# Kernel tuning notes

Hardware: AMD Instinct MI355X
Metric: run time of the kernel (lower is better)

The kernel has to match this reference:

```python
import jax, jax.numpy as jnp
import numpy as np

NUM_GRAPHS = 512
NODES_PER_GRAPH = 152  # hard-coded by reshape(-1, 152*C) in the original forward
DEG = 8
N = NUM_GRAPHS * NODES_PER_GRAPH          # 77824
E = NUM_GRAPHS * NODES_PER_GRAPH * DEG    # 622592
F_IN = 128
HID = 32
HEADS = 6
C = HID * HEADS                           # 192
EPS = 1e-5
NEG_SLOPE = 0.2


def setup_inputs() -> dict:
    key = jax.random.key(0)
    ks = jax.random.split(key, 20)
    x = jax.random.normal(ks[0], (N, F_IN), dtype=jnp.float32)
    # edges are intra-graph: local indices in [0,152) + per-graph offset
    src_l = jax.random.randint(ks[1], (E,), 0, NODES_PER_GRAPH)
    dst_l = jax.random.randint(ks[2], (E,), 0, NODES_PER_GRAPH)
    offs = (jnp.arange(E) // (NODES_PER_GRAPH * DEG)) * NODES_PER_GRAPH
    edge_index = jnp.stack([src_l + offs, dst_l + offs]).astype(jnp.int32)
    batch = (jnp.arange(N) // NODES_PER_GRAPH).astype(jnp.int32)

    def g(k, shape, s=0.05):
        return jax.random.normal(k, shape, dtype=jnp.float32) * s

    return {
        "x": x, "edge_index": edge_index, "batch": batch,
        # GATConv 1: in=128 -> heads=6, d_head=32, concat -> 192
        "W1": g(ks[3], (F_IN, C)), "a_src1": g(ks[4], (HEADS, HID)),
        "a_dst1": g(ks[5], (HEADS, HID)), "b1": jnp.zeros((C,), jnp.float32),
        # GATConv 2: in=192 -> 192
        "W2": g(ks[6], (C, C)), "a_src2": g(ks[7], (HEADS, HID)),
        "a_dst2": g(ks[8], (HEADS, HID)), "b2": jnp.zeros((C,), jnp.float32),
        # GraphNorm 1 / 2: weight, bias, mean_scale (all init like PyG: 1,0,1)
        "gw1": jnp.ones((C,), jnp.float32), "gb1": jnp.zeros((C,), jnp.float32),
        "gms1": jnp.ones((C,), jnp.float32),
        "gw2": jnp.ones((C,), jnp.float32), "gb2": jnp.zeros((C,), jnp.float32),
        "gms2": jnp.ones((C,), jnp.float32),
    }


def _gat_conv(x, W, a_src, a_dst, bias, src, dst):
    # PyG GATConv (concat=True, negative_slope=0.2, add_self_loops already in src/dst)
    h = (x @ W).reshape(N, HEADS, HID)                      # [N,H,D]
    al_s = jnp.einsum('nhd,hd->nh', h, a_src)               # [N,H]
    al_d = jnp.einsum('nhd,hd->nh', h, a_dst)
    e = jax.nn.leaky_relu(al_s[src] + al_d[dst], NEG_SLOPE)  # [E',H]
    # segment softmax over incoming edges of each dst node
    m = jax.ops.segment_max(e, dst, num_segments=N)
    ex = jnp.exp(e - m[dst])
    denom = jax.ops.segment_sum(ex, dst, num_segments=N)
    alpha = ex / denom[dst]                                  # [E',H]
    out = jax.ops.segment_sum(alpha[:, :, None] * h[src], dst, num_segments=N)
    return out.reshape(N, C) + bias


def _graph_norm(x, batch, w, b, ms):
    # PyG GraphNorm: x - mean_scale*mean, normalized by per-graph std
    cnt = jax.ops.segment_sum(jnp.ones((N, 1), x.dtype), batch, num_segments=NUM_GRAPHS)
    mean = jax.ops.segment_sum(x, batch, num_segments=NUM_GRAPHS) / cnt
    out = x - mean[batch] * ms
    var = jax.ops.segment_sum(out * out, batch, num_segments=NUM_GRAPHS) / cnt
    return out / jnp.sqrt(var[batch] + EPS) * w + b


def reference(x, edge_index, batch, W1, a_src1, a_dst1, b1, W2, a_src2, a_dst2, b2,
              gw1, gb1, gms1, gw2, gb2, gms2):
    # add self loops (PyG GATConv default)
    loops = jnp.arange(N, dtype=edge_index.dtype)
    src = jnp.concatenate([edge_index[0], loops])
    dst = jnp.concatenate([edge_index[1], loops])

    h = _gat_conv(x, W1, a_src1, a_dst1, b1, src, dst)
    h = jax.nn.elu(h)
    h = _graph_norm(h, batch, gw1, gb1, gms1)
    # dropout p=0.5 is identity in eval mode
    h = _gat_conv(h, W2, a_src2, a_dst2, b2, src, dst)
    h = jax.nn.elu(h)
    h = _graph_norm(h, batch, gw2, gb2, gms2)
    out = h.reshape(-1, NODES_PER_GRAPH * C)  # [512, 152*192]
    return out  # original returns (x, embedding) where embedding is x itself
```

## Files before the change

kernel.cpp:

```cpp
#include <hip/hip_runtime.h>
#include <stdint.h>

#define NGRAPH 512
#define NPG    152
#define NNODES (NGRAPH*NPG)
#define DEG    8
#define EPG    (NPG*DEG)
#define NEDGE  (NNODES*DEG)
#define CCH    192
#define HEADS  6
#define HID    32
#define NSEG   (NPG+EPG)
#define HSTR   36
#define CNTP   160

typedef __attribute__((ext_vector_type(8))) short short8v;
typedef __attribute__((ext_vector_type(4))) float f32x4;
typedef __attribute__((ext_vector_type(4))) unsigned short ushort4v;

__device__ __forceinline__ unsigned short f2bf(float f){
  union { float f; uint32_t u; } x; x.f = f;
  uint32_t u = x.u;
  return (unsigned short)((u + 0x7fffu + ((u >> 16) & 1u)) >> 16);
}
__device__ __forceinline__ float bitsf(uint32_t b){
  union { uint32_t u; float f; } x; x.u = b; return x.f;
}
__device__ __forceinline__ void gload_lds16(const void* g, void* l){
  __builtin_amdgcn_global_load_lds((const __attribute__((address_space(1))) void*)g,
                                   (__attribute__((address_space(3))) void*)l, 16, 0, 0);
}

__global__ void wprep_all(const float* __restrict__ W1, const float* __restrict__ W2,
                          unsigned short* __restrict__ Wt1, unsigned short* __restrict__ Wt2){
  int idx = blockIdx.x*256 + threadIdx.x;
  if (idx < CCH*128){
    int c = idx >> 7, k = idx & 127;
    Wt1[idx] = f2bf(W1[k*CCH + c]);
  } else if (idx < CCH*(128+192)){
    int j = idx - CCH*128;
    int c = j/192, k = j - c*192;
    Wt2[j] = f2bf(W2[k*CCH + c]);
  }
}

__global__ __launch_bounds__(256) void csr_build(const int* __restrict__ esrc,
    const int* __restrict__ edst, unsigned short* __restrict__ gsrc,
    int* __restrict__ gcnt){
  __shared__ int cnt[256];
  __shared__ int woff[NPG];
  __shared__ __align__(16) unsigned short slots[NSEG];
  const int t = threadIdx.x, g = blockIdx.x, base = g*NPG;

  cnt[t] = (t < NPG) ? 1 : 0;
  __syncthreads();

  int es[5], ed[5];
  #pragma unroll
  for (int u=0;u<5;u++){
    int i = t + u*256;
    if (i < EPG){
      es[u] = esrc[g*EPG + i] - base;
      ed[u] = edst[g*EPG + i] - base;
      atomicAdd(&cnt[ed[u]], 1);
    }
  }
  __syncthreads();
  for (int off=1; off<256; off<<=1){
    int a = cnt[t];
    int b = (t>=off) ? cnt[t-off] : 0;
    __syncthreads();
    cnt[t] = a + b;
    __syncthreads();
  }
  if (t < NPG){
    int st = (t==0) ? 0 : cnt[t-1];
    woff[t] = st;
    gcnt[g*CNTP + t] = st;
  } else if (t < CNTP){
    gcnt[g*CNTP + t] = NSEG;
  }
  __syncthreads();
  #pragma unroll
  for (int u=0;u<5;u++){
    int i = t + u*256;
    if (i < EPG){
      int pos = atomicAdd(&woff[ed[u]], 1);
      slots[pos] = (unsigned short)es[u];
    }
  }
  if (t < NPG){
    int pos = atomicAdd(&woff[t], 1);
    slots[pos] = (unsigned short)t;
  }
  __syncthreads();
  for (int i=t; i<NSEG/8; i+=256)
    *(int4*)(gsrc + (size_t)g*NSEG + i*8) = *(const int4*)&slots[i*8];
}

template<int K, bool A_BF16>
__global__ __launch_bounds__(256) void gemm_mfma(const void* __restrict__ Ap,
    const unsigned short* __restrict__ Bt, unsigned short* __restrict__ H){
  __shared__ unsigned short lA[64*K];
  __shared__ unsigned short lB[96*K];
  const int t  = threadIdx.x;
  const int m0 = blockIdx.x*64, c0 = blockIdx.y*96;

  if (A_BF16){
    const unsigned short* A = (const unsigned short*)Ap + (size_t)m0*K;
    const int CH = 64*K/8;
    for (int i=t; i<CH; i+=256){
      int o   = i*16;
      int row = o / (2*K);
      int db  = o - row*(2*K);
      int sc  = (db>>4) ^ (row&7);
      gload_lds16(A + (size_t)row*K + sc*8, lA + (size_t)(i-(t&63))*8);
    }
  } else {
    const float* A = (const float*)Ap;
    const int KC = K/8;
    for (int i=t; i<64*KC; i+=256){
      int row = i/KC, c8 = i - row*KC;
      const float* p = A + (size_t)(m0+row)*K + c8*8;
      float4 v0 = *(const float4*)p;
      float4 v1 = *(const float4*)(p+4);
      short8v pk;
      pk[0]=(short)f2bf(v0.x); pk[1]=(short)f2bf(v0.y); pk[2]=(short)f2bf(v0.z); pk[3]=(short)f2bf(v0.w);
      pk[4]=(short)f2bf(v1.x); pk[5]=(short)f2bf(v1.y); pk[6]=(short)f2bf(v1.z); pk[7]=(short)f2bf(v1.w);
      *(short8v*)((char*)lA + row*(2*K) + ((c8*16) ^ ((row&7)<<4))) = pk;
    }
  }
  {
    const unsigned short* Bg = Bt + (size_t)c0*K;
    const int CH = 96*K/8;
    for (int i=t; i<CH; i+=256){
      int o   = i*16;
      int row = o / (2*K);
      int db  = o - row*(2*K);
      int sc  = (db>>4) ^ (row&7);
      gload_lds16(Bg + (size_t)row*K + sc*8, lB + (size_t)(i-(t&63))*8);
    }
  }
  __syncthreads();

  const int wid = t>>6, l = t&63;
  const int wr = wid>>1, wc = wid&1;
  const int r16 = l&15, kq = l>>4;
  f32x4 acc[2][3] = {};
  #pragma unroll
  for (int kk=0; kk<K/32; kk++){
    const int chunk = kk*4 + kq;
    short8v af[2], bf[3];
    #pragma unroll
    for (int m=0;m<2;m++){
      int row = wr*32 + m*16 + r16;
      af[m] = *(const short8v*)((const char*)lA + row*(2*K) + ((chunk*16) ^ ((row&7)<<4)));
    }
    #pragma unroll
    for (int n=0;n<3;n++){
      int col = wc*48 + n*16 + r16;
      bf[n] = *(const short8v*)((const char*)lB + col*(2*K) + ((chunk*16) ^ ((col&7)<<4)));
    }
    #pragma unroll
    for (int m=0;m<2;m++)
      #pragma unroll
      for (int n=0;n<3;n++)
        acc[m][n] = __builtin_amdgcn_mfma_f32_16x16x32_bf16(af[m], bf[n], acc[m][n], 0,0,0);
  }
  const int crow = (l>>4)*4;
  #pragma unroll
  for (int m=0;m<2;m++){
    #pragma unroll
    for (int n=0;n<3;n++){
      int colg = c0 + wc*48 + n*16 + r16;
      #pragma unroll
      for (int r=0;r<4;r++){
        int rowg = m0 + wr*32 + m*16 + crow + r;
        H[(size_t)rowg*CCH + colg] = f2bf(acc[m][n][r]);
      }
    }
  }
}

template<bool OUT_BF16>
__global__ __launch_bounds__(256) void gat_edge(
    const unsigned short* __restrict__ H,
    const unsigned short* __restrict__ gsrc, const int* __restrict__ gcnt,
    const float* __restrict__ a_src, const float* __restrict__ a_dst,
    const float* __restrict__ bias, const float* __restrict__ gw,
    const float* __restrict__ gb, const float* __restrict__ gms,
    void* __restrict__ OUTp)
{
  __shared__ float hN[NPG*HSTR];
  __shared__ float als[NPG], ald[NPG];
  __shared__ __align__(16) unsigned short lsrc[NSEG];
  __shared__ __align__(16) int lcnt[CNTP];
  __shared__ float4 ps[8][8];
  __shared__ float4 mred4[8], vred4[8];

  const int t    = threadIdx.x;
  const int g    = blockIdx.x & 511;
  const int hd   = blockIdx.x >> 9;
  const int base = g*NPG;
  const int lane32 = t & 31, grp = t >> 5;

  {
    const unsigned short* gs = gsrc + (size_t)g*NSEG;
    for (int i=t; i<NSEG/8; i+=256)
      gload_lds16(gs + i*8, lsrc + (size_t)(i-(t&63))*8);
    const int* gc = gcnt + (size_t)g*CNTP;
    if (t < CNTP/4)
      gload_lds16(gc + t*4, lcnt + (size_t)(t-(t&63))*4);
  }

  const int c8c = t&3, nb = t>>2;
  const int ab = hd*HID + c8c*8;
  const float4 avs0 = *(const float4*)&a_src[ab];
  const float4 avs1 = *(const float4*)&a_src[ab+4];
  const float4 avd0 = *(const float4*)&a_dst[ab];
  const float4 avd1 = *(const float4*)&a_dst[ab+4];
  #pragma unroll
  for (int it=0; it<3; it++){
    int n = nb + it*64;
    if (n < NPG){
      int4 v = *(const int4*)(H + (size_t)(base+n)*CCH + hd*HID + c8c*8);
      uint32_t w0=(uint32_t)v.x, w1=(uint32_t)v.y, w2=(uint32_t)v.z, w3=(uint32_t)v.w;
      float4 lo = { bitsf(w0<<16), bitsf(w0&0xffff0000u), bitsf(w1<<16), bitsf(w1&0xffff0000u) };
      float4 hi = { bitsf(w2<<16), bitsf(w2&0xffff0000u), bitsf(w3<<16), bitsf(w3&0xffff0000u) };
      float* dst = &hN[n*HSTR + c8c*8];
      *(float4*)dst = lo;
      *(float4*)(dst+4) = hi;
      float s1 = lo.x*avs0.x + lo.y*avs0.y + lo.z*avs0.z + lo.w*avs0.w
               + hi.x*avs1.x + hi.y*avs1.y + hi.z*avs1.z + hi.w*avs1.w;
      float s2 = lo.x*avd0.x + lo.y*avd0.y + lo.z*avd0.z + lo.w*avd0.w
               + hi.x*avd1.x + hi.y*avd1.y + hi.z*avd1.z + hi.w*avd1.w;
      s1 += __shfl_xor(s1, 1); s1 += __shfl_xor(s1, 2);
      s2 += __shfl_xor(s2, 1); s2 += __shfl_xor(s2, 2);
      if (c8c == 0){ als[n] = s1; ald[n] = s2; }
    }
  }
  __syncthreads();

  const int sub = (lane32>>3)&3;
  const int c8  = lane32&7;
  const int o   = grp*4 + sub;
  float4 acc[5]; float den[5]; int stq[5], lnq[5]; float aldn[5];
  #pragma unroll
  for (int q=0;q<5;q++){
    int n = o + q*32;
    int st=0, en=0; float ad=0.f;
    if (n < NPG){ st = lcnt[n]; en = lcnt[n+1]; ad = ald[n]; }
    stq[q]=st; lnq[q]=en-st; aldn[q]=ad;
    acc[q] = float4{0.f,0.f,0.f,0.f}; den[q]=0.f;
  }
  #pragma unroll
  for (int q=0;q<5;q++){
    int st=stq[q], len=lnq[q];
    float ad = aldn[q];
    int rounds = (len+3)>>2;
    for (int r=0;r<rounds;++r){
      #pragma unroll
      for (int u=0;u<4;u++){
        int j = r*4+u;
        int idx = st + ((j<len)? j : 0);
        int s = (int)lsrc[idx];
        float e = als[s] + ad;
        e = (e>0.f) ? e : 0.2f*e;
        float ex = __expf(e);
        if (j>=len) ex = 0.f;
        const float4 hv = *(const float4*)&hN[s*HSTR + c8*4];
        den[q] += ex;
        acc[q].x = fmaf(ex, hv.x, acc[q].x);
        acc[q].y = fmaf(ex, hv.y, acc[q].y);
        acc[q].z = fmaf(ex, hv.z, acc[q].z);
        acc[q].w = fmaf(ex, hv.w, acc[q].w);
      }
    }
  }

  const int cb = hd*HID + c8*4;
  const float4 bs4 = *(const float4*)&bias[cb];
  const float4 gw4 = *(const float4*)&gw[cb];
  const float4 gb4 = *(const float4*)&gb[cb];
  const float4 ms4 = *(const float4*)&gms[cb];

  float4 outv[5];
  float4 psum = {0.f,0.f,0.f,0.f};
  #pragma unroll
  for (int q=0;q<5;q++){
    int n = o + q*32;
    float4 x = {0.f,0.f,0.f,0.f};
    if (n < NPG){
      float inv = 1.f/den[q];
      x.x = acc[q].x*inv + bs4.x;  x.y = acc[q].y*inv + bs4.y;
      x.z = acc[q].z*inv + bs4.z;  x.w = acc[q].w*inv + bs4.w;
      x.x = (x.x>0.f)?x.x:(__expf(x.x)-1.f);
      x.y = (x.y>0.f)?x.y:(__expf(x.y)-1.f);
      x.z = (x.z>0.f)?x.z:(__expf(x.z)-1.f);
      x.w = (x.w>0.f)?x.w:(__expf(x.w)-1.f);
      psum.x+=x.x; psum.y+=x.y; psum.z+=x.z; psum.w+=x.w;
    }
    outv[q]=x;
  }
  psum.x += __shfl_xor(psum.x, 8, 32); psum.y += __shfl_xor(psum.y, 8, 32);
  psum.z += __shfl_xor(psum.z, 8, 32); psum.w += __shfl_xor(psum.w, 8, 32);
  psum.x += __shfl_xor(psum.x,16, 32); psum.y += __shfl_xor(psum.y,16, 32);
  psum.z += __shfl_xor(psum.z,16, 32); psum.w += __shfl_xor(psum.w,16, 32);
  if (sub==0) ps[grp][c8] = psum;
  __syncthreads();
  if (t < 8){
    float4 m = {0.f,0.f,0.f,0.f};
    #pragma unroll
    for (int q=0;q<8;q++){ float4 v=ps[q][t]; m.x+=v.x; m.y+=v.y; m.z+=v.z; m.w+=v.w; }
    m.x*=(1.f/152.f); m.y*=(1.f/152.f); m.z*=(1.f/152.f); m.w*=(1.f/152.f);
    mred4[t] = m;
  }
  __syncthreads();
  const float4 mean4 = mred4[c8];
  float4 v2 = {0.f,0.f,0.f,0.f};
  #pragma unroll
  for (int q=0;q<5;q++){
    int n = o + q*32;
    if (n < NPG){
      outv[q].x -= mean4.x*ms4.x; outv[q].y -= mean4.y*ms4.y;
      outv[q].z -= mean4.z*ms4.z; outv[q].w -= mean4.w*ms4.w;
      v2.x = fmaf(outv[q].x,outv[q].x,v2.x); v2.y = fmaf(outv[q].y,outv[q].y,v2.y);
      v2.z = fmaf(outv[q].z,outv[q].z,v2.z); v2.w = fmaf(outv[q].w,outv[q].w,v2.w);
    }
  }
  v2.x += __shfl_xor(v2.x, 8, 32); v2.y += __shfl_xor(v2.y, 8, 32);
  v2.z += __shfl_xor(v2.z, 8, 32); v2.w += __shfl_xor(v2.w, 8, 32);
  v2.x += __shfl_xor(v2.x,16, 32); v2.y += __shfl_xor(v2.y,16, 32);
  v2.z += __shfl_xor(v2.z,16, 32); v2.w += __shfl_xor(v2.w,16, 32);
  if (sub==0) ps[grp][c8] = v2;
  __syncthreads();
  if (t < 8){
    float4 s = {0.f,0.f,0.f,0.f};
    #pragma unroll
    for (int q=0;q<8;q++){ float4 v=ps[q][t]; s.x+=v.x; s.y+=v.y; s.z+=v.z; s.w+=v.w; }
    float4 rv;
    rv.x = rsqrtf(s.x*(1.f/152.f)+1e-5f); rv.y = rsqrtf(s.y*(1.f/152.f)+1e-5f);
    rv.z = rsqrtf(s.z*(1.f/152.f)+1e-5f); rv.w = rsqrtf(s.w*(1.f/152.f)+1e-5f);
    vred4[t] = rv;
  }
  __syncthreads();
  const float4 rs4 = vred4[c8];
  #pragma unroll
  for (int q=0;q<5;q++){
    int n = o + q*32;
    if (n < NPG){
      float4 x = outv[q];
      x.x = x.x*rs4.x*gw4.x + gb4.x;  x.y = x.y*rs4.y*gw4.y + gb4.y;
      x.z = x.z*rs4.z*gw4.z + gb4.z;  x.w = x.w*rs4.w*gw4.w + gb4.w;
      size_t oidx = (size_t)(base+n)*CCH + cb;
      if (OUT_BF16){
        ushort4v pk = { f2bf(x.x), f2bf(x.y), f2bf(x.z), f2bf(x.w) };
        *(ushort4v*)((unsigned short*)OUTp + oidx) = pk;
      } else {
        *(float4*)((float*)OUTp + oidx) = x;
      }
    }
  }
}

extern "C" void kernel_launch(void* const* d_in, const int* in_sizes, int n_in,
                              void* d_out, int out_size, void* d_ws, size_t ws_size,
                              hipStream_t stream){
  (void)in_sizes; (void)n_in; (void)out_size; (void)ws_size;
  const float* x    = (const float*)d_in[0];
  const int*   ei   = (const int*)  d_in[1];
  const float* W1   = (const float*)d_in[3];
  const float* as1  = (const float*)d_in[4];
  const float* ad1  = (const float*)d_in[5];
  const float* b1   = (const float*)d_in[6];
  const float* W2   = (const float*)d_in[7];
  const float* as2  = (const float*)d_in[8];
  const float* ad2  = (const float*)d_in[9];
  const float* b2   = (const float*)d_in[10];
  const float* gw1  = (const float*)d_in[11];
  const float* gb1  = (const float*)d_in[12];
  const float* gms1 = (const float*)d_in[13];
  const float* gw2  = (const float*)d_in[14];
  const float* gb2  = (const float*)d_in[15];
  const float* gms2 = (const float*)d_in[16];
  const int* esrc = ei;
  const int* edst = ei + NEDGE;

  char* ws = (char*)d_ws;
  unsigned short* Hbuf = (unsigned short*)ws;
  unsigned short* Obuf = (unsigned short*)(ws + (size_t)NNODES*CCH*2);
  unsigned short* Wt1  = (unsigned short*)(ws + (size_t)NNODES*CCH*4);
  unsigned short* Wt2  = Wt1 + CCH*128;
  unsigned short* gsrc = Wt2 + CCH*192;
  int*            gcnt = (int*)(gsrc + (size_t)NGRAPH*NSEG);

  csr_build<<<NGRAPH, 256, 0, stream>>>(esrc, edst, gsrc, gcnt);
  wprep_all<<<(CCH*(128+192)+255)/256, 256, 0, stream>>>(W1, W2, Wt1, Wt2);

  gemm_mfma<128,false><<<dim3(NNODES/64,2), 256, 0, stream>>>((const void*)x, Wt1, Hbuf);
  gat_edge<true><<<NGRAPH*HEADS, 256, 0, stream>>>(Hbuf, gsrc, gcnt, as1, ad1, b1, gw1, gb1, gms1, (void*)Obuf);
  gemm_mfma<192,true><<<dim3(NNODES/64,2), 256, 0, stream>>>((const void*)Obuf, Wt2, Hbuf);
  gat_edge<false><<<NGRAPH*HEADS, 256, 0, stream>>>(Hbuf, gsrc, gcnt, as2, ad2, b2, gw2, gb2, gms2, d_out);
}
```

Before: 232.8 us.

## Aggregate GAT attention as dense per-graph MFMA matmul over packed edge weights

Replaces the per-node CSR gather loop with a dense approach. Each graph's 152x152 attention matrix is scattered into LDS as bf16, with duplicate edges merged into a multiplicity count during preprocessing, and then multiplied by the transposed head features using MFMA. A ones column supplies the softmax denominator. Block size doubles to 512 and the edge list is stored as packed src/mult/dst words. The goal is to remove latency-bound scalar gathers, at the cost of extra LDS zeroing, bf16 rounding of the attention weights, and a large LDS footprint that limits occupancy.

New measurement: 283.9 us. 1.22x slower.

```diff
diff --git a/kernel.cpp b/kernel.cpp
--- a/kernel.cpp
+++ b/kernel.cpp
@@ -11,8 +11,7 @@
 #define HEADS  6
 #define HID    32
 #define NSEG   (NPG+EPG)
-#define HSTR   36
-#define CNTP   160
+#define PST    168
 
 typedef __attribute__((ext_vector_type(8))) short short8v;
 typedef __attribute__((ext_vector_type(4))) float f32x4;
@@ -44,13 +43,12 @@
   }
 }
 
-__global__ __launch_bounds__(256) void csr_build(const int* __restrict__ esrc,
-    const int* __restrict__ edst, unsigned short* __restrict__ gsrc,
-    int* __restrict__ gcnt){
+__global__ __launch_bounds__(256) void pack_build(const int* __restrict__ esrc,
+    const int* __restrict__ edst, unsigned int* __restrict__ gpack){
   __shared__ int cnt[256];
   __shared__ int woff[NPG];
-  __shared__ __align__(16) unsigned short slots[NSEG];
-  const int t = threadIdx.x, g = blockIdx.x, base = g*NPG;
+  __shared__ unsigned short slots[NSEG];
+  const int g = blockIdx.x, t = threadIdx.x, base = g*NPG;
 
   cnt[t] = (t < NPG) ? 1 : 0;
   __syncthreads();
@@ -59,9 +57,10 @@
   #pragma unroll
   for (int u=0;u<5;u++){
     int i = t + u*256;
+    es[u] = -1; ed[u] = -1;
     if (i < EPG){
-      es[u] = esrc[g*EPG + i] - base;
-      ed[u] = edst[g*EPG + i] - base;
+      es[u] = esrc[g*EPG+i] - base;
+      ed[u] = edst[g*EPG+i] - base;
       atomicAdd(&cnt[ed[u]], 1);
     }
   }
@@ -73,18 +72,11 @@
     cnt[t] = a + b;
     __syncthreads();
   }
-  if (t < NPG){
-    int st = (t==0) ? 0 : cnt[t-1];
-    woff[t] = st;
-    gcnt[g*CNTP + t] = st;
-  } else if (t < CNTP){
-    gcnt[g*CNTP + t] = NSEG;
-  }
+  if (t < NPG) woff[t] = (t==0) ? 0 : cnt[t-1];
   __syncthreads();
   #pragma unroll
   for (int u=0;u<5;u++){
-    int i = t + u*256;
-    if (i < EPG){
+    if (ed[u] >= 0){
       int pos = atomicAdd(&woff[ed[u]], 1);
       slots[pos] = (unsigned short)es[u];
     }
@@ -94,8 +86,22 @@
     slots[pos] = (unsigned short)t;
   }
   __syncthreads();
-  for (int i=t; i<NSEG/8; i+=256)
-    *(int4*)(gsrc + (size_t)g*NSEG + i*8) = *(const int4*)&slots[i*8];
+  if (t < NPG){
+    int st = (t==0) ? 0 : cnt[t-1], en = cnt[t];
+    unsigned int* out = gpack + (size_t)g*NSEG;
+    int m = st;
+    for (int j=st; j<en; j++){
+      int s = (int)slots[j];
+      bool first = true;
+      for (int k=st; k<j; k++) if ((int)slots[k]==s){ first=false; break; }
+      if (first){
+        int mult = 1;
+        for (int k=j+1; k<en; k++) if ((int)slots[k]==s) mult++;
+        out[m++] = (unsigned)s | ((unsigned)mult<<8) | ((unsigned)t<<16);
+      }
+    }
+    for (; m<en; m++) out[m] = (152u<<16);
+  }
 }
 
 template<int K, bool A_BF16>
@@ -183,35 +189,35 @@
 }
 
 template<bool OUT_BF16>
-__global__ __launch_bounds__(256) void gat_edge(
+__global__ __launch_bounds__(512) void gat_fused(
     const unsigned short* __restrict__ H,
-    const unsigned short* __restrict__ gsrc, const int* __restrict__ gcnt,
+    const unsigned int* __restrict__ gpack,
     const float* __restrict__ a_src, const float* __restrict__ a_dst,
     const float* __restrict__ bias, const float* __restrict__ gw,
     const float* __restrict__ gb, const float* __restrict__ gms,
     void* __restrict__ OUTp)
 {
-  __shared__ float hN[NPG*HSTR];
-  __shared__ float als[NPG], ald[NPG];
-  __shared__ __align__(16) unsigned short lsrc[NSEG];
-  __shared__ __align__(16) int lcnt[CNTP];
-  __shared__ float4 ps[8][8];
+  __shared__ __align__(16) char arena[160*PST*2];
+  __shared__ __align__(16) unsigned short Ht[48*PST];
+  __shared__ __align__(16) unsigned int lpack[NSEG];
+  __shared__ float als[160], ald[160];
+  __shared__ float4 ps[16][8];
   __shared__ float4 mred4[8], vred4[8];
+
+  unsigned short* P = (unsigned short*)arena;
+  float* outf = (float*)arena;
 
   const int t    = threadIdx.x;
   const int g    = blockIdx.x & 511;
   const int hd   = blockIdx.x >> 9;
   const int base = g*NPG;
-  const int lane32 = t & 31, grp = t >> 5;
-
-  {
-    const unsigned short* gs = gsrc + (size_t)g*NSEG;
-    for (int i=t; i<NSEG/8; i+=256)
-      gload_lds16(gs + i*8, lsrc + (size_t)(i-(t&63))*8);
-    const int* gc = gcnt + (size_t)g*CNTP;
-    if (t < CNTP/4)
-      gload_lds16(gc + t*4, lcnt + (size_t)(t-(t&63))*4);
-  }
+
+  if (t < NSEG/4)
+    gload_lds16(gpack + (size_t)g*NSEG + t*4, lpack + (size_t)(t-(t&63))*4);
+  for (int i=t; i<160*PST/8; i+=512) *(int4*)(P  + i*8) = int4{0,0,0,0};
+  for (int i=t; i< 48*PST/8; i+=512) *(int4*)(Ht + i*8) = int4{0,0,0,0};
+  if (t < 8){ als[NPG+t] = 0.f; ald[NPG+t] = 0.f; }
+  __syncthreads();
 
   const int c8c = t&3, nb = t>>2;
   const int ab = hd*HID + c8c*8;
@@ -220,16 +226,18 @@
   const float4 avd0 = *(const float4*)&a_dst[ab];
   const float4 avd1 = *(const float4*)&a_dst[ab+4];
   #pragma unroll
-  for (int it=0; it<3; it++){
-    int n = nb + it*64;
+  for (int it=0; it<2; it++){
+    int n = nb + it*128;
     if (n < NPG){
       int4 v = *(const int4*)(H + (size_t)(base+n)*CCH + hd*HID + c8c*8);
       uint32_t w0=(uint32_t)v.x, w1=(uint32_t)v.y, w2=(uint32_t)v.z, w3=(uint32_t)v.w;
+      unsigned short* hb = Ht + (c8c*8)*PST + n;
+      hb[0*PST]=(unsigned short)(w0&0xffff); hb[1*PST]=(unsigned short)(w0>>16);
+      hb[2*PST]=(unsigned short)(w1&0xffff); hb[3*PST]=(unsigned short)(w1>>16);
+      hb[4*PST]=(unsigned short)(w2&0xffff); hb[5*PST]=(unsigned short)(w2>>16);
+      hb[6*PST]=(unsigned short)(w3&0xffff); hb[7*PST]=(unsigned short)(w3>>16);
       float4 lo = { bitsf(w0<<16), bitsf(w0&0xffff0000u), bitsf(w1<<16), bitsf(w1&0xffff0000u) };
       float4 hi = { bitsf(w2<<16), bitsf(w2&0xffff0000u), bitsf(w3<<16), bitsf(w3&0xffff0000u) };
-      float* dst = &hN[n*HSTR + c8c*8];
-      *(float4*)dst = lo;
-      *(float4*)(dst+4) = hi;
       float s1 = lo.x*avs0.x + lo.y*avs0.y + lo.z*avs0.z + lo.w*avs0.w
                + hi.x*avs1.x + hi.y*avs1.y + hi.z*avs1.z + hi.w*avs1.w;
       float s2 = lo.x*avd0.x + lo.y*avd0.y + lo.z*avd0.z + lo.w*avd0.w
@@ -239,61 +247,77 @@
       if (c8c == 0){ als[n] = s1; ald[n] = s2; }
     }
   }
-  __syncthreads();
-
-  const int sub = (lane32>>3)&3;
-  const int c8  = lane32&7;
-  const int o   = grp*4 + sub;
-  float4 acc[5]; float den[5]; int stq[5], lnq[5]; float aldn[5];
-  #pragma unroll
-  for (int q=0;q<5;q++){
-    int n = o + q*32;
-    int st=0, en=0; float ad=0.f;
-    if (n < NPG){ st = lcnt[n]; en = lcnt[n+1]; ad = ald[n]; }
-    stq[q]=st; lnq[q]=en-st; aldn[q]=ad;
-    acc[q] = float4{0.f,0.f,0.f,0.f}; den[q]=0.f;
-  }
-  #pragma unroll
-  for (int q=0;q<5;q++){
-    int st=stq[q], len=lnq[q];
-    float ad = aldn[q];
-    int rounds = (len+3)>>2;
-    for (int r=0;r<rounds;++r){
+  if (t < NPG) Ht[32*PST + t] = 0x3F80;
+  __syncthreads();
+
+  for (int i=t; i<NSEG; i+=512){
+    unsigned int pk = lpack[i];
+    int s    = (int)(pk & 0xffu);
+    int mult = (int)((pk>>8) & 0xffu);
+    int d    = (int)(pk >> 16);
+    float e = als[s] + ald[d];
+    e = (e>0.f) ? e : 0.2f*e;
+    float ex = (float)mult * __expf(e);
+    P[d*PST + s] = f2bf(ex);
+  }
+  __syncthreads();
+
+  const int wid = t>>6, l = t&63, r16 = l&15, kq = l>>4;
+  f32x4 accs[4] = {};
+  #pragma unroll
+  for (int a=0; a<4; a++){
+    int ti = wid + a*8;
+    if (ti < 30){
+      int nt = (ti >= 20) ? 2 : ((ti >= 10) ? 1 : 0);
+      int mt = ti - nt*10;
       #pragma unroll
-      for (int u=0;u<4;u++){
-        int j = r*4+u;
-        int idx = st + ((j<len)? j : 0);
-        int s = (int)lsrc[idx];
-        float e = als[s] + ad;
-        e = (e>0.f) ? e : 0.2f*e;
-        float ex = __expf(e);
-        if (j>=len) ex = 0.f;
-        const float4 hv = *(const float4*)&hN[s*HSTR + c8*4];
-        den[q] += ex;
-        acc[q].x = fmaf(ex, hv.x, acc[q].x);
-        acc[q].y = fmaf(ex, hv.y, acc[q].y);
-        acc[q].z = fmaf(ex, hv.z, acc[q].z);
-        acc[q].w = fmaf(ex, hv.w, acc[q].w);
+      for (int k=0; k<5; k++){
+        short8v af = *(const short8v*)(P  + (mt*16 + r16)*PST + (k*4 + kq)*8);
+        short8v bf = *(const short8v*)(Ht + (nt*16 + r16)*PST + (k*4 + kq)*8);
+        accs[a] = __builtin_amdgcn_mfma_f32_16x16x32_bf16(af, bf, accs[a], 0,0,0);
       }
     }
   }
-
+  __syncthreads();
+
+  #pragma unroll
+  for (int a=0; a<4; a++){
+    int ti = wid + a*8;
+    if (ti < 30){
+      int nt = (ti >= 20) ? 2 : ((ti >= 10) ? 1 : 0);
+      int mt = ti - nt*10;
+      int col = nt*16 + r16;
+      if (col < 33){
+        #pragma unroll
+        for (int r=0; r<4; r++){
+          int row = mt*16 + kq*4 + r;
+          if (row < NPG) outf[row*36 + col] = accs[a][r];
+        }
+      }
+    }
+  }
+  __syncthreads();
+
+  const int lane32 = t & 31, grp16 = t >> 5;
+  const int sub = lane32 >> 3, c8 = lane32 & 7;
+  const int o = grp16*4 + sub;
   const int cb = hd*HID + c8*4;
   const float4 bs4 = *(const float4*)&bias[cb];
   const float4 gw4 = *(const float4*)&gw[cb];
   const float4 gb4 = *(const float4*)&gb[cb];
   const float4 ms4 = *(const float4*)&gms[cb];
 
-  float4 outv[5];
+  float4 outv[3];
   float4 psum = {0.f,0.f,0.f,0.f};
   #pragma unroll
-  for (int q=0;q<5;q++){
-    int n = o + q*32;
+  for (int q=0; q<3; q++){
+    int n = o + q*64;
     float4 x = {0.f,0.f,0.f,0.f};
     if (n < NPG){
-      float inv = 1.f/den[q];
-      x.x = acc[q].x*inv + bs4.x;  x.y = acc[q].y*inv + bs4.y;
-      x.z = acc[q].z*inv + bs4.z;  x.w = acc[q].w*inv + bs4.w;
+      float inv = 1.f / outf[n*36 + 32];
+      float4 u = *(const float4*)&outf[n*36 + c8*4];
+      x.x = u.x*inv + bs4.x;  x.y = u.y*inv + bs4.y;
+      x.z = u.z*inv + bs4.z;  x.w = u.w*inv + bs4.w;
       x.x = (x.x>0.f)?x.x:(__expf(x.x)-1.f);
       x.y = (x.y>0.f)?x.y:(__expf(x.y)-1.f);
       x.z = (x.z>0.f)?x.z:(__expf(x.z)-1.f);
@@ -306,12 +330,12 @@
   psum.z += __shfl_xor(psum.z, 8, 32); psum.w += __shfl_xor(psum.w, 8, 32);
   psum.x += __shfl_xor(psum.x,16, 32); psum.y += __shfl_xor(psum.y,16, 32);
   psum.z += __shfl_xor(psum.z,16, 32); psum.w += __shfl_xor(psum.w,16, 32);
-  if (sub==0) ps[grp][c8] = psum;
+  if (sub==0 && lane32<8) ps[grp16][c8] = psum;
   __syncthreads();
   if (t < 8){
     float4 m = {0.f,0.f,0.f,0.f};
     #pragma unroll
-    for (int q=0;q<8;q++){ float4 v=ps[q][t]; m.x+=v.x; m.y+=v.y; m.z+=v.z; m.w+=v.w; }
+    for (int q=0;q<16;q++){ float4 v=ps[q][t]; m.x+=v.x; m.y+=v.y; m.z+=v.z; m.w+=v.w; }
     m.x*=(1.f/152.f); m.y*=(1.f/152.f); m.z*=(1.f/152.f); m.w*=(1.f/152.f);
     mred4[t] = m;
   }
@@ -319,8 +343,8 @@
   const float4 mean4 = mred4[c8];
   float4 v2 = {0.f,0.f,0.f,0.f};
   #pragma unroll
-  for (int q=0;q<5;q++){
-    int n = o + q*32;
+  for (int q=0;q<3;q++){
+    int n = o + q*64;
     if (n < NPG){
       outv[q].x -= mean4.x*ms4.x; outv[q].y -= mean4.y*ms4.y;
       outv[q].z -= mean4.z*ms4.z; outv[q].w -= mean4.w*ms4.w;
@@ -332,12 +356,12 @@
   v2.z += __shfl_xor(v2.z, 8, 32); v2.w += __shfl_xor(v2.w, 8, 32);
   v2.x += __shfl_xor(v2.x,16, 32); v2.y += __shfl_xor(v2.y,16, 32);
   v2.z += __shfl_xor(v2.z,16, 32); v2.w += __shfl_xor(v2.w,16, 32);
-  if (sub==0) ps[grp][c8] = v2;
+  if (sub==0 && lane32<8) ps[grp16][c8] = v2;
   __syncthreads();
   if (t < 8){
     float4 s = {0.f,0.f,0.f,0.f};
     #pragma unroll
-    for (int q=0;q<8;q++){ float4 v=ps[q][t]; s.x+=v.x; s.y+=v.y; s.z+=v.z; s.w+=v.w; }
+    for (int q=0;q<16;q++){ float4 v=ps[q][t]; s.x+=v.x; s.y+=v.y; s.z+=v.z; s.w+=v.w; }
     float4 rv;
     rv.x = rsqrtf(s.x*(1.f/152.f)+1e-5f); rv.y = rsqrtf(s.y*(1.f/152.f)+1e-5f);
     rv.z = rsqrtf(s.z*(1.f/152.f)+1e-5f); rv.w = rsqrtf(s.w*(1.f/152.f)+1e-5f);
@@ -346,8 +370,8 @@
   __syncthreads();
   const float4 rs4 = vred4[c8];
   #pragma unroll
-  for (int q=0;q<5;q++){
-    int n = o + q*32;
+  for (int q=0;q<3;q++){
+    int n = o + q*64;
     if (n < NPG){
       float4 x = outv[q];
       x.x = x.x*rs4.x*gw4.x + gb4.x;  x.y = x.y*rs4.y*gw4.y + gb4.y;
@@ -387,18 +411,17 @@
   const int* edst = ei + NEDGE;
 
   char* ws = (char*)d_ws;
-  unsigned short* Hbuf = (unsigned short*)ws;
-  unsigned short* Obuf = (unsigned short*)(ws + (size_t)NNODES*CCH*2);
-  unsigned short* Wt1  = (unsigned short*)(ws + (size_t)NNODES*CCH*4);
-  unsigned short* Wt2  = Wt1 + CCH*128;
-  unsigned short* gsrc = Wt2 + CCH*192;
-  int*            gcnt = (int*)(gsrc + (size_t)NGRAPH*NSEG);
-
-  csr_build<<<NGRAPH, 256, 0, stream>>>(esrc, edst, gsrc, gcnt);
+  unsigned short* Hbuf  = (unsigned short*)ws;
+  unsigned short* Obuf  = (unsigned short*)(ws + (size_t)NNODES*CCH*2);
+  unsigned short* Wt1   = (unsigned short*)(ws + (size_t)NNODES*CCH*4);
+  unsigned short* Wt2   = Wt1 + CCH*128;
+  unsigned int*   gpack = (unsigned int*)(Wt2 + CCH*192);
+
+  pack_build<<<NGRAPH, 256, 0, stream>>>(esrc, edst, gpack);
   wprep_all<<<(CCH*(128+192)+255)/256, 256, 0, stream>>>(W1, W2, Wt1, Wt2);
 
   gemm_mfma<128,false><<<dim3(NNODES/64,2), 256, 0, stream>>>((const void*)x, Wt1, Hbuf);
-  gat_edge<true><<<NGRAPH*HEADS, 256, 0, stream>>>(Hbuf, gsrc, gcnt, as1, ad1, b1, gw1, gb1, gms1, (void*)Obuf);
+  gat_fused<true><<<NGRAPH*HEADS, 512, 0, stream>>>(Hbuf, gpack, as1, ad1, b1, gw1, gb1, gms1, (void*)Obuf);
   gemm_mfma<192,true><<<dim3(NNODES/64,2), 256, 0, stream>>>((const void*)Obuf, Wt2, Hbuf);
-  gat_edge<false><<<NGRAPH*HEADS, 256, 0, stream>>>(Hbuf, gsrc, gcnt, as2, ad2, b2, gw2, gb2, gms2, d_out);
-}
+  gat_fused<false><<<NGRAPH*HEADS, 512, 0, stream>>>(Hbuf, gpack, as2, ad2, b2, gw2, gb2, gms2, d_out);
+}
```
